# Kernel tuning notes

Measured on AMD Instinct MI355X. Metric: run time of the kernel, lower is better.

## Reference

```python
import jax, jax.numpy as jnp
import numpy as np

B, L, D = 16, 512, 768   # batch, seq_len, hidden_size
H = 12                   # encoder attention heads (self_attention_scores)
K = 128                  # num_preserved_tokens
U, NH = 256, 4           # router attention num_units / num_heads


def setup_inputs() -> dict:
    key = jax.random.key(0)
    ks = jax.random.split(key, 8)
    hidden_states = jax.random.normal(ks[0], (B, L, D), dtype=jnp.float32)
    u = jax.random.uniform(ks[1], (B, 1, 1, L))
    attention_mask = jnp.where(u < 0.9, 0.0, -10000.0).astype(jnp.float32)
    self_attention_scores = jax.random.normal(ks[2], (B, H, L, L), dtype=jnp.float32)
    Wq = jax.random.normal(ks[3], (U, D), dtype=jnp.float32) * 0.02
    Wk = jax.random.normal(ks[4], (U, D), dtype=jnp.float32) * 0.02
    Wv = jax.random.normal(ks[5], (U, D), dtype=jnp.float32) * 0.02
    Wo = jax.random.normal(ks[6], (D, U), dtype=jnp.float32) * 0.02
    bo = jnp.zeros((D,), dtype=jnp.float32)
    return {"hidden_states": hidden_states, "attention_mask": attention_mask,
            "self_attention_scores": self_attention_scores,
            "Wq": Wq, "Wk": Wk, "Wv": Wv, "Wo": Wo, "bo": bo}


def reference(hidden_states, attention_mask, self_attention_scores, Wq, Wk, Wv, Wo, bo):
    # sentence summary: softmax over additive mask -> weighted token average
    att = jax.nn.softmax(attention_mask, axis=-1)            # [B,1,1,L]
    sentences = jnp.einsum('bql,bld->bqd', att[:, 0], hidden_states)  # [B,1,D]

    key_padding_mask = attention_mask[:, 0, 0, :] < -10.0    # [B,L] True = masked

    # MyMultiHeadAttention(query=sentences, key=value=hidden_states)
    hd = U // NH
    q = jnp.einsum('bqd,ud->bqu', sentences, Wq)             # [B,1,U]
    k = jnp.einsum('bld,ud->blu', hidden_states, Wk)         # [B,L,U]
    v = jnp.einsum('bld,ud->blu', hidden_states, Wv)         # [B,L,U]
    qh = q.reshape(B, 1, NH, hd).transpose(2, 0, 1, 3)       # [h,B,1,hd]
    kh = k.reshape(B, L, NH, hd).transpose(2, 0, 1, 3)       # [h,B,L,hd]
    vh = v.reshape(B, L, NH, hd).transpose(2, 0, 1, 3)       # [h,B,L,hd]
    # NOTE: original scales by key_dim**0.5 = hidden_size**0.5 (not head dim)
    scores = jnp.einsum('hbqd,hbkd->hbqk', qh, kh) / (D ** 0.5)  # [h,B,1,L]
    scores = jnp.where(key_padding_mask[None, :, None, :], -jnp.inf, scores)
    probs = jax.nn.softmax(scores, axis=-1)
    out_h = jnp.einsum('hbqk,hbkd->hbqd', probs, vh)         # [h,B,1,hd]
    out = out_h.transpose(1, 2, 0, 3).reshape(B, 1, U)       # concat heads
    new_token = jnp.einsum('bqu,du->bqd', out, Wo) + bo      # [B,1,D]

    class_token = hidden_states[:, :1, :]                    # [B,1,D]

    # importance: mean over heads, sum over query positions -> [B,L]
    importance = self_attention_scores.mean(axis=1).sum(axis=1)
    top_idx = jax.lax.top_k(importance, K)[1]                # [B,K]
    # boolean-mask gather preserves original token order -> sort indices
    sorted_idx = jnp.sort(top_idx, axis=-1)                  # [B,K]
    preserved_tokens = jnp.take_along_axis(hidden_states, sorted_idx[:, :, None], axis=1)  # [B,K,D]
    preserved_mask = jnp.take_along_axis(attention_mask[:, 0, 0, :], sorted_idx, axis=1)
    preserved_mask = preserved_mask.reshape(B, 1, 1, K)

    zmask = jnp.zeros((B, 1, 1, 1), dtype=attention_mask.dtype)
    final_token = jnp.concatenate([class_token, preserved_tokens, new_token], axis=1)  # [B,K+2,D]
    final_attention_mask = jnp.concatenate([zmask, preserved_mask, zmask], axis=-1)    # [B,1,1,K+2]
    return final_token, final_attention_mask
```

## Files before the change

kernel.cpp:

```cpp
#include <hip/hip_runtime.h>
#include <math.h>

#define B_ 16
#define L_ 512
#define D_ 768
#define H_ 12
#define K_ 128
#define U_ 256
#define NH_ 4
#define HD_ 64
#define OUTROWS_ 130
#define IMPCH_ 64

__global__ __launch_bounds__(768) void front_kernel(
    const float* __restrict__ sas, const float* __restrict__ hidden,
    const float* __restrict__ mask, float* __restrict__ part,
    float* __restrict__ sent_part) {
  const int t = threadIdx.x;
  if (blockIdx.x < B_ * IMPCH_) {
    __shared__ float4 lbuf[6][128];
    const int b = blockIdx.x >> 6, chunk = blockIdx.x & 63;
    const int col4 = t & 127;
    const int rg = t >> 7;
    const float4* base = (const float4*)sas +
        ((size_t)(b * (H_ * L_) + chunk * 96 + rg * 16)) * 128 + col4;
    float4 a = make_float4(0.f, 0.f, 0.f, 0.f);
    #pragma unroll
    for (int k = 0; k < 16; ++k) {
      float4 v = base[(size_t)k * 128];
      a.x += v.x; a.y += v.y; a.z += v.z; a.w += v.w;
    }
    lbuf[rg][col4] = a;
    __syncthreads();
    if (rg == 0) {
      float4 o = lbuf[0][col4];
      #pragma unroll
      for (int g = 1; g < 6; ++g) {
        float4 v = lbuf[g][col4];
        o.x += v.x; o.y += v.y; o.z += v.z; o.w += v.w;
      }
      const float s = 1.0f / 12.0f;
      o.x *= s; o.y *= s; o.z *= s; o.w *= s;
      ((float4*)part)[((size_t)b * IMPCH_ + chunk) * 128 + col4] = o;
    }
  } else {
    __shared__ float att[L_];
    __shared__ float red_m[12], red_s[12];
    __shared__ float4 cbuf[4][192];
    const int i = blockIdx.x - B_ * IMPCH_;
    const int b = i >> 4, chunk = i & 15;
    const int wave = t >> 6, lane = t & 63;
    const float m = (t < L_) ? mask[b * L_ + t] : -INFINITY;
    float r = m;
    #pragma unroll
    for (int off = 32; off > 0; off >>= 1) r = fmaxf(r, __shfl_down(r, off, 64));
    if (lane == 0) red_m[wave] = r;
    __syncthreads();
    float mx = red_m[0];
    #pragma unroll
    for (int w = 1; w < 12; ++w) mx = fmaxf(mx, red_m[w]);
    const float e = (t < L_) ? expf(m - mx) : 0.f;
    float rs = e;
    #pragma unroll
    for (int off = 32; off > 0; off >>= 1) rs += __shfl_down(rs, off, 64);
    if (lane == 0) red_s[wave] = rs;
    __syncthreads();
    float se = 0.f;
    #pragma unroll
    for (int w = 0; w < 12; ++w) se += red_s[w];
    if (t < L_) att[t] = e / se;
    __syncthreads();
    const int c4 = t % 192, sub = t / 192;
    const int l0 = chunk * 32 + sub * 8;
    const float4* h4 = (const float4*)hidden + ((size_t)b * L_ + l0) * 192 + c4;
    float4 acc = make_float4(0.f, 0.f, 0.f, 0.f);
    #pragma unroll
    for (int ii = 0; ii < 8; ++ii) {
      const float w = att[l0 + ii];
      const float4 hv = h4[(size_t)ii * 192];
      acc.x += w * hv.x; acc.y += w * hv.y; acc.z += w * hv.z; acc.w += w * hv.w;
    }
    cbuf[sub][c4] = acc;
    __syncthreads();
    if (t < 192) {
      float4 o = cbuf[0][t];
      #pragma unroll
      for (int g = 1; g < 4; ++g) {
        const float4 v = cbuf[g][t];
        o.x += v.x; o.y += v.y; o.z += v.z; o.w += v.w;
      }
      ((float4*)sent_part)[((size_t)b * 16 + chunk) * 192 + t] = o;
    }
  }
}

__global__ __launch_bounds__(768) void qproj_topk_kernel(
    const float* __restrict__ sent_part, const float* __restrict__ Wq,
    const float* __restrict__ Wk, float* __restrict__ wqe,
    const float* __restrict__ part, const float* __restrict__ mask,
    const float* __restrict__ hidden, float* __restrict__ out0,
    float* __restrict__ out1, float* __restrict__ outv) {
  __shared__ float s[D_];
  __shared__ float qvh[HD_];
  __shared__ float v[L_];
  __shared__ int lidx[K_];
  __shared__ int wcnt[12];
  const int t = threadIdx.x;
  const int wave = t >> 6, lane = t & 63;

  if (blockIdx.x < 64) {
    const int b = blockIdx.x >> 2, h = blockIdx.x & 3;
    {
      const float* sp = sent_part + (size_t)b * 16 * D_ + t;
      float a = 0.f;
      #pragma unroll
      for (int c = 0; c < 16; ++c) a += sp[(size_t)c * D_];
      s[t] = a;
    }
    __syncthreads();
    for (int u = wave; u < HD_; u += 12) {
      const float* wr = Wq + (size_t)(h * HD_ + u) * D_;
      float acc = 0.f;
      #pragma unroll
      for (int k = 0; k < 12; ++k) {
        const int d = lane + (k << 6);
        acc += wr[d] * s[d];
      }
      #pragma unroll
      for (int o = 32; o > 0; o >>= 1) acc += __shfl_down(acc, o, 64);
      if (lane == 0) qvh[u] = acc;
    }
    __syncthreads();
    {
      float acc = 0.f;
      const float* wk = Wk + (size_t)(h * HD_) * D_ + t;
      #pragma unroll 4
      for (int j = 0; j < HD_; ++j) acc += qvh[j] * wk[(size_t)j * D_];
      wqe[((size_t)b * NH_ + h) * D_ + t] = acc;
    }
  } else {
    const int b = blockIdx.x - 64;
    if (t < U_) outv[b * U_ + t] = 0.f;
    if (t < L_) {
      const float* pp = part + (size_t)b * IMPCH_ * L_ + t;
      float sum = 0.f;
      #pragma unroll 8
      for (int g = 0; g < IMPCH_; ++g) sum += pp[(size_t)g * L_];
      v[t] = sum;
    }
    __syncthreads();
    bool sel = false;
    if (t < L_) {
      const float mv = v[t];
      int cnt = 0;
      #pragma unroll 8
      for (int j = 0; j < L_; ++j) {
        float o = v[j];
        cnt += (o > mv) || (o == mv && j < t);
      }
      sel = cnt < K_;
    }
    const unsigned long long ball = __ballot(sel);
    if (lane == 0) wcnt[wave] = __popcll(ball);
    __syncthreads();
    int base = 0;
    for (int w = 0; w < wave; ++w) base += wcnt[w];
    const int pos = base + __popcll(ball & ((1ull << lane) - 1ull));
    if (sel) {
      lidx[pos] = t;
      out1[b * OUTROWS_ + 1 + pos] = mask[b * L_ + t];
    }
    if (t == 0) {
      out1[b * OUTROWS_ + 0] = 0.f;
      out1[b * OUTROWS_ + OUTROWS_ - 1] = 0.f;
    }
    __syncthreads();
    const float4* hb4 = (const float4*)(hidden + (size_t)b * L_ * D_);
    float4* ob4 = (float4*)(out0 + (size_t)b * OUTROWS_ * D_);
    const int NG = (K_ + 1) * 192;
    for (int i = t; i < NG; i += 768) {
      const int r = i / 192;
      const int c = i - r * 192;
      const int src = (r == 0) ? 0 : lidx[r - 1];
      ob4[r * 192 + c] = hb4[src * 192 + c];
    }
  }
}

__global__ __launch_bounds__(256) void score_kernel(
    const float* __restrict__ hidden, const float* __restrict__ mask,
    const float* __restrict__ wqe, float* __restrict__ scores) {
  __shared__ float4 wq4[NH_ * 192];
  const int b = blockIdx.x, chunk = blockIdx.y, t = threadIdx.x;
  {
    const float4* wsrc = (const float4*)(wqe + (size_t)b * NH_ * D_);
    for (int i = t; i < NH_ * 192; i += 256) wq4[i] = wsrc[i];
  }
  __syncthreads();
  const int wave = t >> 6, lane = t & 63;
  const float scale = 0.03608439182435161f;
  #pragma unroll
  for (int r = 0; r < 8; ++r) {
    const int l = chunk * 32 + wave * 8 + r;
    const float4* hr4 = (const float4*)(hidden + ((size_t)b * L_ + l) * D_);
    float s0 = 0.f, s1 = 0.f, s2 = 0.f, s3 = 0.f;
    #pragma unroll
    for (int jj = 0; jj < 3; ++jj) {
      const int c = lane + 64 * jj;
      const float4 hv = hr4[c];
      const float4 w0 = wq4[0 * 192 + c];
      const float4 w1 = wq4[1 * 192 + c];
      const float4 w2 = wq4[2 * 192 + c];
      const float4 w3 = wq4[3 * 192 + c];
      s0 += hv.x * w0.x + hv.y * w0.y + hv.z * w0.z + hv.w * w0.w;
      s1 += hv.x * w1.x + hv.y * w1.y + hv.z * w1.z + hv.w * w1.w;
      s2 += hv.x * w2.x + hv.y * w2.y + hv.z * w2.z + hv.w * w2.w;
      s3 += hv.x * w3.x + hv.y * w3.y + hv.z * w3.z + hv.w * w3.w;
    }
    #pragma unroll
    for (int o = 32; o > 0; o >>= 1) {
      s0 += __shfl_down(s0, o, 64);
      s1 += __shfl_down(s1, o, 64);
      s2 += __shfl_down(s2, o, 64);
      s3 += __shfl_down(s3, o, 64);
    }
    if (lane == 0) {
      const bool kp = mask[b * L_ + l] < -10.f;
      float* sp = scores + (size_t)b * NH_ * L_ + l;
      sp[0 * L_] = kp ? -INFINITY : s0 * scale;
      sp[1 * L_] = kp ? -INFINITY : s1 * scale;
      sp[2 * L_] = kp ? -INFINITY : s2 * scale;
      sp[3 * L_] = kp ? -INFINITY : s3 * scale;
    }
  }
}

__global__ __launch_bounds__(768) void ctx_outv_kernel(
    const float* __restrict__ hidden, const float* __restrict__ scores,
    const float* __restrict__ Wv, float* __restrict__ outv) {
  __shared__ float pr[NH_][32];
  __shared__ float red_m[NH_][12], red_s[NH_][12];
  __shared__ __align__(16) float ctxs[NH_ * D_];
  const int b = blockIdx.x, chunk = blockIdx.y, t = threadIdx.x;
  const int wave = t >> 6, lane = t & 63;
  const int l0 = chunk * 32;

  float val[NH_];
  #pragma unroll
  for (int h = 0; h < NH_; ++h)
    val[h] = (t < L_) ? scores[((size_t)b * NH_ + h) * L_ + t] : -INFINITY;
  #pragma unroll
  for (int h = 0; h < NH_; ++h) {
    float r = val[h];
    #pragma unroll
    for (int off = 32; off > 0; off >>= 1) r = fmaxf(r, __shfl_down(r, off, 64));
    if (lane == 0) red_m[h][wave] = r;
  }
  __syncthreads();
  float e[NH_];
  #pragma unroll
  for (int h = 0; h < NH_; ++h) {
    float mx = red_m[h][0];
    #pragma unroll
    for (int w = 1; w < 12; ++w) mx = fmaxf(mx, red_m[h][w]);
    e[h] = (t < L_) ? expf(val[h] - mx) : 0.f;
    float rs = e[h];
    #pragma unroll
    for (int off = 32; off > 0; off >>= 1) rs += __shfl_down(rs, off, 64);
    if (lane == 0) red_s[h][wave] = rs;
  }
  __syncthreads();
  if (t >= l0 && t < l0 + 32) {
    #pragma unroll
    for (int h = 0; h < NH_; ++h) {
      float se = 0.f;
      #pragma unroll
      for (int w = 0; w < 12; ++w) se += red_s[h][w];
      pr[h][t - l0] = e[h] / se;
    }
  }
  __syncthreads();

  const int c4 = t % 192, hh = t / 192;
  const float4* h4 = (const float4*)hidden + ((size_t)b * L_ + l0) * 192 + c4;
  float4 acc = make_float4(0.f, 0.f, 0.f, 0.f);
  #pragma unroll 8
  for (int l = 0; l < 32; ++l) {
    const float w = pr[hh][l];
    const float4 hv = h4[(size_t)l * 192];
    acc.x += w * hv.x; acc.y += w * hv.y; acc.z += w * hv.z; acc.w += w * hv.w;
  }
  ((float4*)ctxs)[hh * 192 + c4] = acc;
  __syncthreads();

  for (int hu = wave; hu < U_; hu += 12) {
    const float* wr = Wv + (size_t)hu * D_;
    const float* ch = ctxs + (hu >> 6) * D_;
    float a = 0.f;
    #pragma unroll
    for (int k = 0; k < 12; ++k) {
      const int d = lane + (k << 6);
      a += wr[d] * ch[d];
    }
    #pragma unroll
    for (int off = 32; off > 0; off >>= 1) a += __shfl_down(a, off, 64);
    if (lane == 0) atomicAdd(&outv[b * U_ + hu], a);
  }
}

__global__ __launch_bounds__(192) void newtoken_kernel(
    const float* __restrict__ outv, const float* __restrict__ Wo,
    const float* __restrict__ bo, float* __restrict__ out0) {
  __shared__ float4 ov4[64];
  const int b = blockIdx.x, q = blockIdx.y, t = threadIdx.x;
  const int wave = t >> 6, lane = t & 63;
  if (t < 64) ov4[t] = ((const float4*)(outv + b * U_))[t];
  __syncthreads();
  const int dbase = q * 192 + wave * 64;
  const float4 o = ov4[lane];
  for (int i = 0; i < 64; ++i) {
    const int d = dbase + i;
    const float4 w = ((const float4*)(Wo + (size_t)d * U_))[lane];
    float acc = w.x * o.x + w.y * o.y + w.z * o.z + w.w * o.w;
    #pragma unroll
    for (int off = 32; off > 0; off >>= 1) acc += __shfl_down(acc, off, 64);
    if (lane == 0)
      out0[((size_t)b * OUTROWS_ + (OUTROWS_ - 1)) * D_ + d] = bo[d] + acc;
  }
}

extern "C" void kernel_launch(void* const* d_in, const int* in_sizes, int n_in,
                              void* d_out, int out_size, void* d_ws, size_t ws_size,
                              hipStream_t stream) {
  const float* hidden = (const float*)d_in[0];
  const float* mask   = (const float*)d_in[1];
  const float* sas    = (const float*)d_in[2];
  const float* Wq     = (const float*)d_in[3];
  const float* Wk     = (const float*)d_in[4];
  const float* Wv     = (const float*)d_in[5];
  const float* Wo     = (const float*)d_in[6];
  const float* bo     = (const float*)d_in[7];

  float* out0 = (float*)d_out;
  float* out1 = out0 + (size_t)B_ * OUTROWS_ * D_;

  float* part      = (float*)d_ws;
  float* sent_part = part + (size_t)B_ * IMPCH_ * L_;
  float* wqe       = sent_part + (size_t)B_ * 16 * D_;
  float* scores    = wqe + (size_t)B_ * NH_ * D_;
  float* outv      = scores + (size_t)B_ * NH_ * L_;

  front_kernel<<<B_ * IMPCH_ + B_ * 16, 768, 0, stream>>>(sas, hidden, mask,
                                                          part, sent_part);
  qproj_topk_kernel<<<80, 768, 0, stream>>>(sent_part, Wq, Wk, wqe,
                                            part, mask, hidden, out0, out1, outv);
  score_kernel<<<dim3(B_, 16), 256, 0, stream>>>(hidden, mask, wqe, scores);
  ctx_outv_kernel<<<dim3(B_, 16), 768, 0, stream>>>(hidden, scores, Wv, outv);
  newtoken_kernel<<<dim3(B_, 4), 192, 0, stream>>>(outv, Wo, bo, out0);
}
```

Baseline: 413.2 us.

## Split front kernel, drop Wv atomics, restructure importance and new-token projections

Splits the combined importance/sentence kernel into two launches. The importance reduction now uses 256-thread blocks with a 96-group partial layout and no shared-memory stage. The ctx/Wv projection no longer re-reads Wv from every chunk block with atomics: per-chunk ctx partials go to workspace, and a separate outv kernel reduces them and applies Wv once per batch and head. The new-token projection is rewritten to tile Wo across all batches in shared memory, so each Wo row is read once rather than once per batch. These changes add two kernel launches and extra workspace traffic.

New measurement: 362.9 us. 12.2% less time.

```diff
diff --git a/kernel.cpp b/kernel.cpp
--- a/kernel.cpp
+++ b/kernel.cpp
@@ -10,87 +10,74 @@
 #define NH_ 4
 #define HD_ 64
 #define OUTROWS_ 130
-#define IMPCH_ 64
-
-__global__ __launch_bounds__(768) void front_kernel(
-    const float* __restrict__ sas, const float* __restrict__ hidden,
-    const float* __restrict__ mask, float* __restrict__ part,
+#define IMP_G_ 96
+
+__global__ __launch_bounds__(256) void importance_kernel(
+    const float* __restrict__ scores, float* __restrict__ part) {
+  const int b = blockIdx.y, chunk = blockIdx.x, t = threadIdx.x;
+  const int qcol = t & 127;
+  const int rhalf = t >> 7;
+  const float4* base = (const float4*)scores +
+      ((size_t)(b * (H_ * L_) + chunk * 128 + rhalf)) * 128 + qcol;
+  float4 a = make_float4(0.f, 0.f, 0.f, 0.f);
+  #pragma unroll 8
+  for (int r = 0; r < 64; ++r) {
+    float4 v = base[(size_t)r * 256];
+    a.x += v.x; a.y += v.y; a.z += v.z; a.w += v.w;
+  }
+  const float s = 1.0f / 12.0f;
+  float4 o = make_float4(a.x * s, a.y * s, a.z * s, a.w * s);
+  ((float4*)part)[((size_t)b * IMP_G_ + chunk * 2 + rhalf) * 128 + qcol] = o;
+}
+
+__global__ __launch_bounds__(768) void sent_kernel(
+    const float* __restrict__ hidden, const float* __restrict__ mask,
     float* __restrict__ sent_part) {
-  const int t = threadIdx.x;
-  if (blockIdx.x < B_ * IMPCH_) {
-    __shared__ float4 lbuf[6][128];
-    const int b = blockIdx.x >> 6, chunk = blockIdx.x & 63;
-    const int col4 = t & 127;
-    const int rg = t >> 7;
-    const float4* base = (const float4*)sas +
-        ((size_t)(b * (H_ * L_) + chunk * 96 + rg * 16)) * 128 + col4;
-    float4 a = make_float4(0.f, 0.f, 0.f, 0.f);
-    #pragma unroll
-    for (int k = 0; k < 16; ++k) {
-      float4 v = base[(size_t)k * 128];
-      a.x += v.x; a.y += v.y; a.z += v.z; a.w += v.w;
-    }
-    lbuf[rg][col4] = a;
-    __syncthreads();
-    if (rg == 0) {
-      float4 o = lbuf[0][col4];
-      #pragma unroll
-      for (int g = 1; g < 6; ++g) {
-        float4 v = lbuf[g][col4];
-        o.x += v.x; o.y += v.y; o.z += v.z; o.w += v.w;
-      }
-      const float s = 1.0f / 12.0f;
-      o.x *= s; o.y *= s; o.z *= s; o.w *= s;
-      ((float4*)part)[((size_t)b * IMPCH_ + chunk) * 128 + col4] = o;
-    }
-  } else {
-    __shared__ float att[L_];
-    __shared__ float red_m[12], red_s[12];
-    __shared__ float4 cbuf[4][192];
-    const int i = blockIdx.x - B_ * IMPCH_;
-    const int b = i >> 4, chunk = i & 15;
-    const int wave = t >> 6, lane = t & 63;
-    const float m = (t < L_) ? mask[b * L_ + t] : -INFINITY;
-    float r = m;
-    #pragma unroll
-    for (int off = 32; off > 0; off >>= 1) r = fmaxf(r, __shfl_down(r, off, 64));
-    if (lane == 0) red_m[wave] = r;
-    __syncthreads();
-    float mx = red_m[0];
-    #pragma unroll
-    for (int w = 1; w < 12; ++w) mx = fmaxf(mx, red_m[w]);
-    const float e = (t < L_) ? expf(m - mx) : 0.f;
-    float rs = e;
-    #pragma unroll
-    for (int off = 32; off > 0; off >>= 1) rs += __shfl_down(rs, off, 64);
-    if (lane == 0) red_s[wave] = rs;
-    __syncthreads();
-    float se = 0.f;
-    #pragma unroll
-    for (int w = 0; w < 12; ++w) se += red_s[w];
-    if (t < L_) att[t] = e / se;
-    __syncthreads();
-    const int c4 = t % 192, sub = t / 192;
-    const int l0 = chunk * 32 + sub * 8;
-    const float4* h4 = (const float4*)hidden + ((size_t)b * L_ + l0) * 192 + c4;
-    float4 acc = make_float4(0.f, 0.f, 0.f, 0.f);
-    #pragma unroll
-    for (int ii = 0; ii < 8; ++ii) {
-      const float w = att[l0 + ii];
-      const float4 hv = h4[(size_t)ii * 192];
-      acc.x += w * hv.x; acc.y += w * hv.y; acc.z += w * hv.z; acc.w += w * hv.w;
-    }
-    cbuf[sub][c4] = acc;
-    __syncthreads();
-    if (t < 192) {
-      float4 o = cbuf[0][t];
-      #pragma unroll
-      for (int g = 1; g < 4; ++g) {
-        const float4 v = cbuf[g][t];
-        o.x += v.x; o.y += v.y; o.z += v.z; o.w += v.w;
-      }
-      ((float4*)sent_part)[((size_t)b * 16 + chunk) * 192 + t] = o;
-    }
+  __shared__ float att[L_];
+  __shared__ float red_m[12], red_s[12];
+  __shared__ float4 cbuf[4][192];
+  const int b = blockIdx.x, chunk = blockIdx.y, t = threadIdx.x;
+  const int wave = t >> 6, lane = t & 63;
+  const float m = (t < L_) ? mask[b * L_ + t] : -INFINITY;
+  float r = m;
+  #pragma unroll
+  for (int off = 32; off > 0; off >>= 1) r = fmaxf(r, __shfl_down(r, off, 64));
+  if (lane == 0) red_m[wave] = r;
+  __syncthreads();
+  float mx = red_m[0];
+  #pragma unroll
+  for (int w = 1; w < 12; ++w) mx = fmaxf(mx, red_m[w]);
+  const float e = (t < L_) ? expf(m - mx) : 0.f;
+  float rs = e;
+  #pragma unroll
+  for (int off = 32; off > 0; off >>= 1) rs += __shfl_down(rs, off, 64);
+  if (lane == 0) red_s[wave] = rs;
+  __syncthreads();
+  float se = 0.f;
+  #pragma unroll
+  for (int w = 0; w < 12; ++w) se += red_s[w];
+  if (t < L_) att[t] = e / se;
+  __syncthreads();
+  const int c4 = t % 192, sub = t / 192;
+  const int l0 = chunk * 32 + sub * 8;
+  const float4* h4 = (const float4*)hidden + ((size_t)b * L_ + l0) * 192 + c4;
+  float4 acc = make_float4(0.f, 0.f, 0.f, 0.f);
+  #pragma unroll
+  for (int ii = 0; ii < 8; ++ii) {
+    const float w = att[l0 + ii];
+    const float4 hv = h4[(size_t)ii * 192];
+    acc.x += w * hv.x; acc.y += w * hv.y; acc.z += w * hv.z; acc.w += w * hv.w;
+  }
+  cbuf[sub][c4] = acc;
+  __syncthreads();
+  if (t < 192) {
+    float4 o = cbuf[0][t];
+    #pragma unroll
+    for (int g = 1; g < 4; ++g) {
+      const float4 v = cbuf[g][t];
+      o.x += v.x; o.y += v.y; o.z += v.z; o.w += v.w;
+    }
+    ((float4*)sent_part)[((size_t)b * 16 + chunk) * 192 + t] = o;
   }
 }
 
@@ -99,7 +86,7 @@
     const float* __restrict__ Wk, float* __restrict__ wqe,
     const float* __restrict__ part, const float* __restrict__ mask,
     const float* __restrict__ hidden, float* __restrict__ out0,
-    float* __restrict__ out1, float* __restrict__ outv) {
+    float* __restrict__ out1) {
   __shared__ float s[D_];
   __shared__ float qvh[HD_];
   __shared__ float v[L_];
@@ -140,12 +127,11 @@
     }
   } else {
     const int b = blockIdx.x - 64;
-    if (t < U_) outv[b * U_ + t] = 0.f;
     if (t < L_) {
-      const float* pp = part + (size_t)b * IMPCH_ * L_ + t;
+      const float* pp = part + (size_t)b * IMP_G_ * L_ + t;
       float sum = 0.f;
       #pragma unroll 8
-      for (int g = 0; g < IMPCH_; ++g) sum += pp[(size_t)g * L_];
+      for (int g = 0; g < IMP_G_; ++g) sum += pp[(size_t)g * L_];
       v[t] = sum;
     }
     __syncthreads();
@@ -235,12 +221,11 @@
   }
 }
 
-__global__ __launch_bounds__(768) void ctx_outv_kernel(
+__global__ __launch_bounds__(768) void ctx_prob_kernel(
     const float* __restrict__ hidden, const float* __restrict__ scores,
-    const float* __restrict__ Wv, float* __restrict__ outv) {
+    float* __restrict__ ctx_part) {
   __shared__ float pr[NH_][32];
   __shared__ float red_m[NH_][12], red_s[NH_][12];
-  __shared__ __align__(16) float ctxs[NH_ * D_];
   const int b = blockIdx.x, chunk = blockIdx.y, t = threadIdx.x;
   const int wave = t >> 6, lane = t & 63;
   const int l0 = chunk * 32;
@@ -290,43 +275,59 @@
     const float4 hv = h4[(size_t)l * 192];
     acc.x += w * hv.x; acc.y += w * hv.y; acc.z += w * hv.z; acc.w += w * hv.w;
   }
-  ((float4*)ctxs)[hh * 192 + c4] = acc;
-  __syncthreads();
-
-  for (int hu = wave; hu < U_; hu += 12) {
-    const float* wr = Wv + (size_t)hu * D_;
-    const float* ch = ctxs + (hu >> 6) * D_;
+  ((float4*)ctx_part)[(((size_t)b * 16 + chunk) * NH_ + hh) * 192 + c4] = acc;
+}
+
+__global__ __launch_bounds__(768) void outv_kernel(
+    const float* __restrict__ ctx_part, const float* __restrict__ Wv,
+    float* __restrict__ outv) {
+  __shared__ float ch[D_];
+  const int b = blockIdx.x, h = blockIdx.y, t = threadIdx.x;
+  const int wave = t >> 6, lane = t & 63;
+  {
     float a = 0.f;
+    #pragma unroll
+    for (int c = 0; c < 16; ++c)
+      a += ctx_part[(((size_t)b * 16 + c) * NH_ + h) * D_ + t];
+    ch[t] = a;
+  }
+  __syncthreads();
+  for (int u = wave; u < HD_; u += 12) {
+    const float* wr = Wv + (size_t)(h * HD_ + u) * D_;
+    float acc = 0.f;
     #pragma unroll
     for (int k = 0; k < 12; ++k) {
       const int d = lane + (k << 6);
-      a += wr[d] * ch[d];
-    }
-    #pragma unroll
-    for (int off = 32; off > 0; off >>= 1) a += __shfl_down(a, off, 64);
-    if (lane == 0) atomicAdd(&outv[b * U_ + hu], a);
-  }
-}
-
-__global__ __launch_bounds__(192) void newtoken_kernel(
+      acc += wr[d] * ch[d];
+    }
+    #pragma unroll
+    for (int o = 32; o > 0; o >>= 1) acc += __shfl_down(acc, o, 64);
+    if (lane == 0) outv[b * U_ + h * HD_ + u] = acc;
+  }
+}
+
+__global__ __launch_bounds__(256) void newtoken_ws_kernel(
     const float* __restrict__ outv, const float* __restrict__ Wo,
     const float* __restrict__ bo, float* __restrict__ out0) {
-  __shared__ float4 ov4[64];
-  const int b = blockIdx.x, q = blockIdx.y, t = threadIdx.x;
-  const int wave = t >> 6, lane = t & 63;
-  if (t < 64) ov4[t] = ((const float4*)(outv + b * U_))[t];
-  __syncthreads();
-  const int dbase = q * 192 + wave * 64;
-  const float4 o = ov4[lane];
-  for (int i = 0; i < 64; ++i) {
-    const int d = dbase + i;
-    const float4 w = ((const float4*)(Wo + (size_t)d * U_))[lane];
-    float acc = w.x * o.x + w.y * o.y + w.z * o.z + w.w * o.w;
-    #pragma unroll
-    for (int off = 32; off > 0; off >>= 1) acc += __shfl_down(acc, off, 64);
-    if (lane == 0)
-      out0[((size_t)b * OUTROWS_ + (OUTROWS_ - 1)) * D_ + d] = bo[d] + acc;
-  }
+  __shared__ float ovs[16 * 260];
+  __shared__ float wot[16 * 260];
+  const int d0 = blockIdx.x * 16, t = threadIdx.x;
+  #pragma unroll
+  for (int k = 0; k < 16; ++k) {
+    const int i = t + (k << 8);
+    const int row = i >> 8, u = i & 255;
+    ovs[row * 260 + u] = outv[i];
+    wot[row * 260 + u] = Wo[(size_t)(d0 + row) * U_ + u];
+  }
+  __syncthreads();
+  const int b = t >> 4, dl = t & 15;
+  const float* ov = ovs + b * 260;
+  const float* wr = wot + dl * 260;
+  float acc = 0.f;
+  #pragma unroll 8
+  for (int u = 0; u < U_; ++u) acc += ov[u] * wr[u];
+  const int d = d0 + dl;
+  out0[((size_t)b * OUTROWS_ + (OUTROWS_ - 1)) * D_ + d] = bo[d] + acc;
 }
 
 extern "C" void kernel_launch(void* const* d_in, const int* in_sizes, int n_in,
@@ -345,16 +346,18 @@
   float* out1 = out0 + (size_t)B_ * OUTROWS_ * D_;
 
   float* part      = (float*)d_ws;
-  float* sent_part = part + (size_t)B_ * IMPCH_ * L_;
-  float* wqe       = sent_part + (size_t)B_ * 16 * D_;
+  float* sent_part = part + (size_t)B_ * IMP_G_ * L_;
+  float* ctx_part  = sent_part + (size_t)B_ * 16 * D_;
+  float* wqe       = ctx_part + (size_t)B_ * 16 * NH_ * D_;
   float* scores    = wqe + (size_t)B_ * NH_ * D_;
   float* outv      = scores + (size_t)B_ * NH_ * L_;
 
-  front_kernel<<<B_ * IMPCH_ + B_ * 16, 768, 0, stream>>>(sas, hidden, mask,
-                                                          part, sent_part);
+  importance_kernel<<<dim3(48, B_), 256, 0, stream>>>(sas, part);
+  sent_kernel<<<dim3(B_, 16), 768, 0, stream>>>(hidden, mask, sent_part);
   qproj_topk_kernel<<<80, 768, 0, stream>>>(sent_part, Wq, Wk, wqe,
-                                            part, mask, hidden, out0, out1, outv);
+                                            part, mask, hidden, out0, out1);
   score_kernel<<<dim3(B_, 16), 256, 0, stream>>>(hidden, mask, wqe, scores);
-  ctx_outv_kernel<<<dim3(B_, 16), 768, 0, stream>>>(hidden, scores, Wv, outv);
-  newtoken_kernel<<<dim3(B_, 4), 192, 0, stream>>>(outv, Wo, bo, out0);
-}
+  ctx_prob_kernel<<<dim3(B_, 16), 768, 0, stream>>>(hidden, scores, ctx_part);
+  outv_kernel<<<dim3(B_, NH_), 768, 0, stream>>>(ctx_part, Wv, outv);
+  newtoken_ws_kernel<<<48, 256, 0, stream>>>(outv, Wo, bo, out0);
+}
```
